# Optimization experiments

Hardware: AMD Instinct MI355X
Metric: run time of the kernel (lower is better)

## Reference

```python
import jax, jax.numpy as jnp
import numpy as np

N_FEATURES = 128
N_ACTIONS = 16
HIDDEN = 256
BATCH = 4096
IN_DIM = N_FEATURES + N_ACTIONS  # 144


def setup_inputs() -> dict:
    key = jax.random.key(0)
    k1, k2, k3, k4 = jax.random.split(key, 4)
    f_t = jax.random.normal(k1, (BATCH, N_FEATURES), dtype=jnp.float32)
    a_t = jax.random.normal(k2, (BATCH, N_ACTIONS), dtype=jnp.float32)
    # Stacked per-feature MLP params (one small MLP per output feature).
    W1 = jax.random.normal(k3, (N_FEATURES, IN_DIM, HIDDEN), dtype=jnp.float32) / np.sqrt(IN_DIM)
    b1 = jnp.zeros((N_FEATURES, HIDDEN), dtype=jnp.float32)
    W2 = jax.random.normal(k4, (N_FEATURES, HIDDEN), dtype=jnp.float32) / np.sqrt(HIDDEN)
    b2 = jnp.zeros((N_FEATURES,), dtype=jnp.float32)
    return {"f_t": f_t, "a_t": a_t, "W1": W1, "b1": b1, "W2": W2, "b2": b2}


def reference(f_t, a_t, W1, b1, W2, b2):
    # fa_t: [B, F+A] shared input to all per-feature models
    fa_t = jnp.concatenate((f_t, a_t), axis=1)
    # Grouped GEMM replacing parallel_apply over n_features tiny MLPs:
    # h: [M, B, H]
    h = jax.nn.relu(jnp.einsum('bi,mih->mbh', fa_t, W1) + b1[:, None, :])
    # out: [B, M]  (each model emits a single scalar per example)
    out = jnp.einsum('mbh,mh->bm', h, W2) + b2[None, :]
    # skip_connection=True, additional=False, all=False -> add f_t
    return out + f_t
```

## Files before the change

### kernel.cpp

```cpp
#include <hip/hip_runtime.h>
#include <hip/hip_bf16.h>

#define BATCH   4096
#define NF      128
#define NA      16
#define IN_DIM  144
#define KP      160
#define KF      192
#define HID     256

typedef __attribute__((ext_vector_type(8))) short bf16x8;
typedef __attribute__((ext_vector_type(4))) float f32x4;
typedef unsigned int u32;

__device__ __forceinline__ void gl_lds16(const void* gsrc, void* ldst) {
    __builtin_amdgcn_global_load_lds(
        (const __attribute__((address_space(1))) u32*)gsrc,
        (__attribute__((address_space(3))) u32*)ldst, 16, 0, 0);
}

__global__ void convert_fa(const float* __restrict__ f_t,
                           const float* __restrict__ a_t,
                           __hip_bfloat16* __restrict__ fab) {
    int c = blockIdx.x * blockDim.x + threadIdx.x;
    const int total = BATCH * (KF / 8);
    if (c >= total) return;
    int row = c / 24;
    int cc = c - row * 24;
    union { ushort us[8]; uint4 q; } pk;
#pragma unroll
    for (int j = 0; j < 8; ++j) {
        int k = cc * 8 + j;
        float v;
        if (k < NF)            v = f_t[(size_t)row * NF + k];
        else if (k < IN_DIM)   v = a_t[(size_t)row * NA + (k - NF)];
        else if (k == IN_DIM)  v = 1.0f;
        else                   v = 0.0f;
        __hip_bfloat16 h = __float2bfloat16(v);
        pk.us[j] = *(ushort*)&h;
    }
    int pc = cc ^ (row & 7);
    *(uint4*)(fab + (size_t)row * KF + pc * 8) = pk.q;
}

__global__ void convert_w1t(const float* __restrict__ W1,
                            const float* __restrict__ b1,
                            __hip_bfloat16* __restrict__ w1t) {
    __shared__ float tile[16][HID];
    int bid = blockIdx.x;
    int m = bid / 10;
    int kc = bid - m * 10;
    int t = threadIdx.x;
    int k0 = kc * 16;
    if (kc < 9) {
#pragma unroll
        for (int i = 0; i < 16; ++i)
            tile[i][t] = W1[((size_t)m * IN_DIM + (k0 + i)) * HID + t];
        __syncthreads();
        union { ushort us[16]; uint4 q[2]; } pk;
#pragma unroll
        for (int i = 0; i < 16; ++i) {
            __hip_bfloat16 h = __float2bfloat16(tile[i][t]);
            pk.us[i] = *(ushort*)&h;
        }
        uint4* dst = (uint4*)(w1t + ((size_t)m * HID + t) * KP + k0);
        dst[0] = pk.q[0];
        dst[1] = pk.q[1];
    } else {
        union { ushort us[8]; uint4 q; } pk;
#pragma unroll
        for (int j = 0; j < 8; ++j) pk.us[j] = 0;
        __hip_bfloat16 hb = __float2bfloat16(b1[(size_t)m * HID + t]);
        pk.us[0] = *(ushort*)&hb;
        uint4 z = {0u, 0u, 0u, 0u};
        uint4* dst = (uint4*)(w1t + ((size_t)m * HID + t) * KP + IN_DIM);
        dst[0] = pk.q;
        dst[1] = z;
    }
}

__global__ __launch_bounds__(256) void fused_mlp(
        const __hip_bfloat16* __restrict__ fab,
        const __hip_bfloat16* __restrict__ w1t,
        const float* __restrict__ W2,
        const float* __restrict__ b2,
        const float* __restrict__ f_t,
        float* __restrict__ out) {
    __shared__ __align__(16) __hip_bfloat16 Abuf[2][64 * KF];
    __shared__ __align__(16) float partial[2][4][64];

    const int bid = blockIdx.x;
    const int m     = bid & 127;
    const int slice = bid >> 7;
    const int row_base = slice * 1024;
    const int t = threadIdx.x;
    const int w = t >> 6;
    const int lane = t & 63;
    const int lrow = lane & 15;
    const int g = lane >> 4;
    const int xr = (lrow & 7) << 4;

    bf16x8 bfrag[4][5];
#pragma unroll
    for (int hi = 0; hi < 4; ++hi) {
        const int col = w * 64 + hi * 16 + lrow;
        const __hip_bfloat16* wp = w1t + ((size_t)m * HID + col) * KP + g * 8;
#pragma unroll
        for (int ks = 0; ks < 5; ++ks)
            bfrag[hi][ks] = *(const bf16x8*)(wp + ks * 32);
    }
    f32x4 w2v[4];
#pragma unroll
    for (int hi = 0; hi < 4; ++hi)
        w2v[hi] = *(const f32x4*)(W2 + (size_t)m * HID + w * 64 + hi * 16 + g * 4);
    const float b2v = b2[m];

    {
        const char* src = (const char*)(fab + (size_t)row_base * KF);
        char* dst = (char*)&Abuf[0][0];
#pragma unroll
        for (int i = 0; i < 6; ++i)
            gl_lds16(src + (size_t)(t + i * 256) * 16, dst + (t + i * 256) * 16);
    }
    __syncthreads();

    for (int tile = 0; tile < 16; ++tile) {
        const int cur = tile & 1;
        const int r0 = row_base + tile * 64;

        if (tile < 15) {
            const char* src = (const char*)(fab + (size_t)(r0 + 64) * KF);
            char* dst = (char*)&Abuf[cur ^ 1][0];
#pragma unroll
            for (int i = 0; i < 6; ++i)
                gl_lds16(src + (size_t)(t + i * 256) * 16, dst + (t + i * 256) * 16);
        }
        float skipv = 0.0f;
        if (t < 64) skipv = f_t[(size_t)(r0 + t) * NF + m];

        f32x4 acc[4][4];
#pragma unroll
        for (int hi = 0; hi < 4; ++hi)
#pragma unroll
            for (int bj = 0; bj < 4; ++bj)
                acc[hi][bj] = (f32x4){0.f, 0.f, 0.f, 0.f};

        const char* ab = (const char*)&Abuf[cur][0];
#pragma unroll
        for (int ks = 0; ks < 5; ++ks) {
            bf16x8 a[4];
#pragma unroll
            for (int bj = 0; bj < 4; ++bj) {
                int off = (bj * 16 + lrow) * 384 + ((ks * 64 + g * 16) ^ xr);
                a[bj] = *(const bf16x8*)(ab + off);
            }
#pragma unroll
            for (int hi = 0; hi < 4; ++hi)
#pragma unroll
                for (int bj = 0; bj < 4; ++bj)
                    acc[hi][bj] = __builtin_amdgcn_mfma_f32_16x16x32_bf16(
                        bfrag[hi][ks], a[bj], acc[hi][bj], 0, 0, 0);
        }

        float sarr[4];
#pragma unroll
        for (int bj = 0; bj < 4; ++bj) {
            float s = 0.f;
#pragma unroll
            for (int hi = 0; hi < 4; ++hi)
#pragma unroll
                for (int r = 0; r < 4; ++r) {
                    float h = acc[hi][bj][r];
                    h = h > 0.f ? h : 0.f;
                    s = fmaf(h, w2v[hi][r], s);
                }
            s += __shfl_xor(s, 16, 64);
            s += __shfl_xor(s, 32, 64);
            sarr[bj] = s;
        }
        float sv = (g == 0) ? sarr[0] : (g == 1) ? sarr[1]
                 : (g == 2) ? sarr[2] : sarr[3];
        partial[cur][w][lane] = sv;

        __syncthreads();
        if (t < 64) {
            float v = partial[cur][0][t] + partial[cur][1][t]
                    + partial[cur][2][t] + partial[cur][3][t]
                    + b2v + skipv;
            out[(size_t)(r0 + t) * NF + m] = v;
        }
    }
}

extern "C" void kernel_launch(void* const* d_in, const int* in_sizes, int n_in,
                              void* d_out, int out_size, void* d_ws, size_t ws_size,
                              hipStream_t stream) {
    const float* f_t = (const float*)d_in[0];
    const float* a_t = (const float*)d_in[1];
    const float* W1  = (const float*)d_in[2];
    const float* b1  = (const float*)d_in[3];
    const float* W2  = (const float*)d_in[4];
    const float* b2  = (const float*)d_in[5];
    float* out = (float*)d_out;

    __hip_bfloat16* w1t = (__hip_bfloat16*)d_ws;
    __hip_bfloat16* fab = (__hip_bfloat16*)((char*)d_ws + (size_t)NF * HID * KP * 2);

    hipLaunchKernelGGL(convert_w1t, dim3(NF * 10), dim3(256), 0, stream, W1, b1, w1t);
    hipLaunchKernelGGL(convert_fa, dim3((BATCH * (KF / 8) + 255) / 256), dim3(256),
                       0, stream, f_t, a_t, fab);
    hipLaunchKernelGGL(fused_mlp, dim3(512), dim3(256), 0, stream,
                       fab, w1t, W2, b2, f_t, out);
}
```

Measured before the change: 60.73 us.

## Merge conversion kernels and double the GEMM grid to 1024 blocks

Merges the W1 transpose and activation-conversion kernels into a single launch, removing one kernel launch and its gap. Halves the rows each fused_mlp block handles (512 instead of 1024), so the grid grows to 1024 blocks and fills the 256 CUs better. In exchange, each block's per-block B-fragment load from W1 is amortised over fewer tiles. Also splits the ReLU/W2 dot product into four independent FMA chains to shorten the dependency chain.

After: 60.58 us. Within noise of the previous version (-0.2%).

```diff
diff --git a/kernel.cpp b/kernel.cpp
--- a/kernel.cpp
+++ b/kernel.cpp
@@ -19,63 +19,64 @@
         (__attribute__((address_space(3))) u32*)ldst, 16, 0, 0);
 }
 
-__global__ void convert_fa(const float* __restrict__ f_t,
-                           const float* __restrict__ a_t,
-                           __hip_bfloat16* __restrict__ fab) {
-    int c = blockIdx.x * blockDim.x + threadIdx.x;
-    const int total = BATCH * (KF / 8);
-    if (c >= total) return;
-    int row = c / 24;
-    int cc = c - row * 24;
-    union { ushort us[8]; uint4 q; } pk;
-#pragma unroll
-    for (int j = 0; j < 8; ++j) {
-        int k = cc * 8 + j;
-        float v;
-        if (k < NF)            v = f_t[(size_t)row * NF + k];
-        else if (k < IN_DIM)   v = a_t[(size_t)row * NA + (k - NF)];
-        else if (k == IN_DIM)  v = 1.0f;
-        else                   v = 0.0f;
-        __hip_bfloat16 h = __float2bfloat16(v);
-        pk.us[j] = *(ushort*)&h;
-    }
-    int pc = cc ^ (row & 7);
-    *(uint4*)(fab + (size_t)row * KF + pc * 8) = pk.q;
-}
-
-__global__ void convert_w1t(const float* __restrict__ W1,
+__global__ void convert_all(const float* __restrict__ W1,
                             const float* __restrict__ b1,
-                            __hip_bfloat16* __restrict__ w1t) {
-    __shared__ float tile[16][HID];
-    int bid = blockIdx.x;
-    int m = bid / 10;
-    int kc = bid - m * 10;
-    int t = threadIdx.x;
-    int k0 = kc * 16;
-    if (kc < 9) {
-#pragma unroll
-        for (int i = 0; i < 16; ++i)
-            tile[i][t] = W1[((size_t)m * IN_DIM + (k0 + i)) * HID + t];
-        __syncthreads();
-        union { ushort us[16]; uint4 q[2]; } pk;
-#pragma unroll
-        for (int i = 0; i < 16; ++i) {
-            __hip_bfloat16 h = __float2bfloat16(tile[i][t]);
-            pk.us[i] = *(ushort*)&h;
-        }
-        uint4* dst = (uint4*)(w1t + ((size_t)m * HID + t) * KP + k0);
-        dst[0] = pk.q[0];
-        dst[1] = pk.q[1];
+                            const float* __restrict__ f_t,
+                            const float* __restrict__ a_t,
+                            __hip_bfloat16* __restrict__ w1t,
+                            __hip_bfloat16* __restrict__ fab) {
+    const int bid = blockIdx.x;
+    const int t = threadIdx.x;
+    if (bid < 1280) {
+        __shared__ float tile[16][HID];
+        int m = bid / 10;
+        int kc = bid - m * 10;
+        int k0 = kc * 16;
+        if (kc < 9) {
+#pragma unroll
+            for (int i = 0; i < 16; ++i)
+                tile[i][t] = W1[((size_t)m * IN_DIM + (k0 + i)) * HID + t];
+            __syncthreads();
+            union { ushort us[16]; uint4 q[2]; } pk;
+#pragma unroll
+            for (int i = 0; i < 16; ++i) {
+                __hip_bfloat16 h = __float2bfloat16(tile[i][t]);
+                pk.us[i] = *(ushort*)&h;
+            }
+            uint4* dst = (uint4*)(w1t + ((size_t)m * HID + t) * KP + k0);
+            dst[0] = pk.q[0];
+            dst[1] = pk.q[1];
+        } else {
+            union { ushort us[8]; uint4 q; } pk;
+#pragma unroll
+            for (int j = 0; j < 8; ++j) pk.us[j] = 0;
+            __hip_bfloat16 hb = __float2bfloat16(b1[(size_t)m * HID + t]);
+            pk.us[0] = *(ushort*)&hb;
+            uint4 z = {0u, 0u, 0u, 0u};
+            uint4* dst = (uint4*)(w1t + ((size_t)m * HID + t) * KP + IN_DIM);
+            dst[0] = pk.q;
+            dst[1] = z;
+        }
     } else {
+        int c = (bid - 1280) * 256 + t;
+        const int total = BATCH * (KF / 8);
+        if (c >= total) return;
+        int row = c / 24;
+        int cc = c - row * 24;
         union { ushort us[8]; uint4 q; } pk;
 #pragma unroll
-        for (int j = 0; j < 8; ++j) pk.us[j] = 0;
-        __hip_bfloat16 hb = __float2bfloat16(b1[(size_t)m * HID + t]);
-        pk.us[0] = *(ushort*)&hb;
-        uint4 z = {0u, 0u, 0u, 0u};
-        uint4* dst = (uint4*)(w1t + ((size_t)m * HID + t) * KP + IN_DIM);
-        dst[0] = pk.q;
-        dst[1] = z;
+        for (int j = 0; j < 8; ++j) {
+            int k = cc * 8 + j;
+            float v;
+            if (k < NF)            v = f_t[(size_t)row * NF + k];
+            else if (k < IN_DIM)   v = a_t[(size_t)row * NA + (k - NF)];
+            else if (k == IN_DIM)  v = 1.0f;
+            else                   v = 0.0f;
+            __hip_bfloat16 h = __float2bfloat16(v);
+            pk.us[j] = *(ushort*)&h;
+        }
+        int pc = cc ^ (row & 7);
+        *(uint4*)(fab + (size_t)row * KF + pc * 8) = pk.q;
     }
 }
 
@@ -92,7 +93,7 @@
     const int bid = blockIdx.x;
     const int m     = bid & 127;
     const int slice = bid >> 7;
-    const int row_base = slice * 1024;
+    const int row_base = slice * 512;
     const int t = threadIdx.x;
     const int w = t >> 6;
     const int lane = t & 63;
@@ -124,11 +125,11 @@
     }
     __syncthreads();
 
-    for (int tile = 0; tile < 16; ++tile) {
+    for (int tile = 0; tile < 8; ++tile) {
         const int cur = tile & 1;
         const int r0 = row_base + tile * 64;
 
-        if (tile < 15) {
+        if (tile < 7) {
             const char* src = (const char*)(fab + (size_t)(r0 + 64) * KF);
             char* dst = (char*)&Abuf[cur ^ 1][0];
 #pragma unroll
@@ -165,15 +166,19 @@
         float sarr[4];
 #pragma unroll
         for (int bj = 0; bj < 4; ++bj) {
-            float s = 0.f;
-#pragma unroll
-            for (int hi = 0; hi < 4; ++hi)
-#pragma unroll
-                for (int r = 0; r < 4; ++r) {
-                    float h = acc[hi][bj][r];
-                    h = h > 0.f ? h : 0.f;
-                    s = fmaf(h, w2v[hi][r], s);
-                }
+            float sr0 = 0.f, sr1 = 0.f, sr2 = 0.f, sr3 = 0.f;
+#pragma unroll
+            for (int hi = 0; hi < 4; ++hi) {
+                float h0 = acc[hi][bj][0]; h0 = h0 > 0.f ? h0 : 0.f;
+                float h1 = acc[hi][bj][1]; h1 = h1 > 0.f ? h1 : 0.f;
+                float h2 = acc[hi][bj][2]; h2 = h2 > 0.f ? h2 : 0.f;
+                float h3 = acc[hi][bj][3]; h3 = h3 > 0.f ? h3 : 0.f;
+                sr0 = fmaf(h0, w2v[hi][0], sr0);
+                sr1 = fmaf(h1, w2v[hi][1], sr1);
+                sr2 = fmaf(h2, w2v[hi][2], sr2);
+                sr3 = fmaf(h3, w2v[hi][3], sr3);
+            }
+            float s = (sr0 + sr1) + (sr2 + sr3);
             s += __shfl_xor(s, 16, 64);
             s += __shfl_xor(s, 32, 64);
             sarr[bj] = s;
@@ -206,9 +211,8 @@
     __hip_bfloat16* w1t = (__hip_bfloat16*)d_ws;
     __hip_bfloat16* fab = (__hip_bfloat16*)((char*)d_ws + (size_t)NF * HID * KP * 2);
 
-    hipLaunchKernelGGL(convert_w1t, dim3(NF * 10), dim3(256), 0, stream, W1, b1, w1t);
-    hipLaunchKernelGGL(convert_fa, dim3((BATCH * (KF / 8) + 255) / 256), dim3(256),
-                       0, stream, f_t, a_t, fab);
-    hipLaunchKernelGGL(fused_mlp, dim3(512), dim3(256), 0, stream,
+    hipLaunchKernelGGL(convert_all, dim3(1664), dim3(256), 0, stream,
+                       W1, b1, f_t, a_t, w1t, fab);
+    hipLaunchKernelGGL(fused_mlp, dim3(1024), dim3(256), 0, stream,
                        fab, w1t, W2, b2, f_t, out);
 }
```
